# Performance work log

Hardware: AMD Instinct MI355X
Metric: run time of the kernel (lower is better)

Reference implementation:

```python
import jax, jax.numpy as jnp
import numpy as np

B, T, D = 4, 2048, 1024
H, DK = 8, 64
EPS = 1e-6

def _xavier(key, shape):
    fan_in, fan_out = shape[1], shape[0]
    lim = float(np.sqrt(6.0 / (fan_in + fan_out)))
    return jax.random.uniform(key, shape, jnp.float32, -lim, lim)

def setup_inputs() -> dict:
    key = jax.random.key(0)
    ks = jax.random.split(key, 7)
    x = jax.random.normal(ks[0], (B, T, D), jnp.float32)
    W_Q = _xavier(ks[1], (H * DK, D))
    W_K = _xavier(ks[2], (H * DK, D))
    W_V = _xavier(ks[3], (H * DK, D))
    W_g_w = _xavier(ks[4], (H * DK, D))
    W_g_b = jax.random.normal(ks[5], (H * DK,), jnp.float32) * 0.02
    W_O = _xavier(ks[6], (D, H * DK))
    decay_log = jnp.zeros((H,), jnp.float32)
    return {"x": x, "W_Q": W_Q, "W_K": W_K, "W_V": W_V,
            "W_g_w": W_g_w, "W_g_b": W_g_b, "W_O": W_O,
            "decay_log": decay_log}

def _phi(u):
    # ELU + 1 feature map (positive)
    return jax.nn.elu(u) + 1.0

def reference(x, W_Q, W_K, W_V, W_g_w, W_g_b, W_O, decay_log):
    b, t, d = x.shape
    q = _phi((x @ W_Q.T).reshape(b, t, H, DK))
    k = _phi((x @ W_K.T).reshape(b, t, H, DK))
    v = (x @ W_V.T).reshape(b, t, H, DK)
    gamma = jax.nn.sigmoid(decay_log)           # [H]
    g4 = gamma[None, :, None, None]             # [1,H,1,1]
    g3 = gamma[None, :, None]                   # [1,H,1]

    # time-major for scan: [T,B,H,DK]
    qT = jnp.moveaxis(q, 1, 0)
    kT = jnp.moveaxis(k, 1, 0)
    vT = jnp.moveaxis(v, 1, 0)

    S0 = jnp.zeros((b, H, DK, DK), x.dtype)
    z0 = jnp.zeros((b, H, DK), x.dtype)

    def step(carry, inp):
        S, z = carry
        qt, kt, vt = inp
        S = g4 * S + jnp.einsum('bhi,bhj->bhij', kt, vt)
        z = g3 * z + kt
        num = jnp.einsum('bhij,bhi->bhj', S, qt)
        den = jnp.sum(z * qt, axis=-1, keepdims=True) + EPS
        return (S, z), num / den

    _, ys = jax.lax.scan(step, (S0, z0), (qT, kT, vT))  # ys: [T,B,H,DK]
    outputs = jnp.moveaxis(ys, 0, 1)                    # [B,T,H,DK]

    gate = jax.nn.sigmoid(x @ W_g_w.T + W_g_b).reshape(b, t, H, DK)
    y = (outputs * gate).reshape(b, t, H * DK)
    return y @ W_O.T
```

## Files before the change

kernel.cpp:

```cpp
#include <hip/hip_runtime.h>
#include <cstdint>
#include <cstddef>

#define B_   4
#define T_   2048
#define D_   1024
#define H_   8
#define DK_  64
#define HD_  512
#define CH_  64
#define NC_  32
#define EPS_ 1e-6f

typedef __attribute__((ext_vector_type(4))) float f32x4;
typedef __attribute__((ext_vector_type(8))) short s16x8;

__device__ __forceinline__ unsigned short f2bf(float f) {
    unsigned int x = __float_as_uint(f);
    unsigned int r = (x + 0x7FFFu + ((x >> 16) & 1u)) >> 16;
    return (unsigned short)r;
}
__device__ __forceinline__ float bf2f(unsigned short u) {
    return __uint_as_float(((unsigned int)u) << 16);
}
__device__ __forceinline__ void ld4(const float* p, float* o) {
    float4 v = *(const float4*)p; o[0]=v.x; o[1]=v.y; o[2]=v.z; o[3]=v.w;
}

__global__ void k_f32_to_bf16(const float* __restrict__ in, unsigned short* __restrict__ out, int n4) {
    int i = blockIdx.x * blockDim.x + threadIdx.x;
    if (i < n4) {
        float4 v = ((const float4*)in)[i];
        ushort4 o;
        o.x = f2bf(v.x); o.y = f2bf(v.y); o.z = f2bf(v.z); o.w = f2bf(v.w);
        ((ushort4*)out)[i] = o;
    }
}

#define GT_M 128
#define GT_N 128
#define GBK  64
#define LDA  72

__global__ __launch_bounds__(256) void k_gemm_qkvg(
    const unsigned short* __restrict__ xb,
    const unsigned short* __restrict__ wqb, const unsigned short* __restrict__ wkb,
    const unsigned short* __restrict__ wvb, const unsigned short* __restrict__ wgb,
    const float* __restrict__ bias,
    unsigned short* __restrict__ qo, unsigned short* __restrict__ ko,
    unsigned short* __restrict__ vo, unsigned short* __restrict__ go)
{
    __shared__ unsigned short As[GT_M * LDA];
    __shared__ unsigned short Bs[GT_N * LDA];
    const int tid = threadIdx.x;
    const int which = blockIdx.x >> 2;
    const int nb    = blockIdx.x & 3;
    const int m0    = blockIdx.y * GT_M;
    const int n0    = nb * GT_N;
    const unsigned short* Wp = (which == 0) ? wqb : (which == 1) ? wkb : (which == 2) ? wvb : wgb;
    unsigned short* Op       = (which == 0) ? qo  : (which == 1) ? ko  : (which == 2) ? vo  : go;
    const int K = D_;

    const int lane = tid & 63, wave = tid >> 6;
    const int wm = (wave >> 1) * 64, wn = (wave & 1) * 64;
    const int r16 = lane & 15, quad = lane >> 4;

    f32x4 acc[4][4];
    #pragma unroll
    for (int a = 0; a < 4; a++)
        #pragma unroll
        for (int b = 0; b < 4; b++) acc[a][b] = 0.0f;

    for (int ko_ = 0; ko_ < K; ko_ += GBK) {
        #pragma unroll
        for (int i = 0; i < 4; i++) {
            int id = i * 256 + tid;
            int row = id >> 3, seg = id & 7;
            *(uint4*)&As[row * LDA + seg * 8] =
                *(const uint4*)(xb + (size_t)(m0 + row) * K + ko_ + seg * 8);
            *(uint4*)&Bs[row * LDA + seg * 8] =
                *(const uint4*)(Wp + (size_t)(n0 + row) * K + ko_ + seg * 8);
        }
        __syncthreads();
        #pragma unroll
        for (int kk = 0; kk < GBK; kk += 32) {
            s16x8 af[4], bf[4];
            #pragma unroll
            for (int mt = 0; mt < 4; mt++)
                af[mt] = *(const s16x8*)&As[(wm + mt * 16 + r16) * LDA + kk + quad * 8];
            #pragma unroll
            for (int nt = 0; nt < 4; nt++)
                bf[nt] = *(const s16x8*)&Bs[(wn + nt * 16 + r16) * LDA + kk + quad * 8];
            #pragma unroll
            for (int mt = 0; mt < 4; mt++)
                #pragma unroll
                for (int nt = 0; nt < 4; nt++)
                    acc[mt][nt] = __builtin_amdgcn_mfma_f32_16x16x32_bf16(af[mt], bf[nt], acc[mt][nt], 0, 0, 0);
        }
        __syncthreads();
    }
    #pragma unroll
    for (int mt = 0; mt < 4; mt++) {
        #pragma unroll
        for (int nt = 0; nt < 4; nt++) {
            int col = n0 + wn + nt * 16 + r16;
            float bv = (which == 3) ? bias[col] : 0.0f;
            #pragma unroll
            for (int r = 0; r < 4; r++) {
                int row = m0 + wm + mt * 16 + quad * 4 + r;
                float v = acc[mt][nt][r];
                if (which <= 1)      v = (v > 0.0f) ? v + 1.0f : __builtin_expf(v);
                else if (which == 3) v = 1.0f / (1.0f + __builtin_expf(-(v + bv)));
                Op[(size_t)row * HD_ + col] = f2bf(v);
            }
        }
    }
}

__global__ __launch_bounds__(256) void k_gemm_out(
    const unsigned short* __restrict__ ogb, const unsigned short* __restrict__ wob,
    float* __restrict__ y)
{
    __shared__ unsigned short As[GT_M * LDA];
    __shared__ unsigned short Bs[GT_N * LDA];
    const int tid = threadIdx.x;
    const int m0 = blockIdx.y * GT_M;
    const int n0 = blockIdx.x * GT_N;
    const int K = HD_;

    const int lane = tid & 63, wave = tid >> 6;
    const int wm = (wave >> 1) * 64, wn = (wave & 1) * 64;
    const int r16 = lane & 15, quad = lane >> 4;

    f32x4 acc[4][4];
    #pragma unroll
    for (int a = 0; a < 4; a++)
        #pragma unroll
        for (int b = 0; b < 4; b++) acc[a][b] = 0.0f;

    for (int ko_ = 0; ko_ < K; ko_ += GBK) {
        #pragma unroll
        for (int i = 0; i < 4; i++) {
            int id = i * 256 + tid;
            int row = id >> 3, seg = id & 7;
            *(uint4*)&As[row * LDA + seg * 8] =
                *(const uint4*)(ogb + (size_t)(m0 + row) * K + ko_ + seg * 8);
            *(uint4*)&Bs[row * LDA + seg * 8] =
                *(const uint4*)(wob + (size_t)(n0 + row) * K + ko_ + seg * 8);
        }
        __syncthreads();
        #pragma unroll
        for (int kk = 0; kk < GBK; kk += 32) {
            s16x8 af[4], bf[4];
            #pragma unroll
            for (int mt = 0; mt < 4; mt++)
                af[mt] = *(const s16x8*)&As[(wm + mt * 16 + r16) * LDA + kk + quad * 8];
            #pragma unroll
            for (int nt = 0; nt < 4; nt++)
                bf[nt] = *(const s16x8*)&Bs[(wn + nt * 16 + r16) * LDA + kk + quad * 8];
            #pragma unroll
            for (int mt = 0; mt < 4; mt++)
                #pragma unroll
                for (int nt = 0; nt < 4; nt++)
                    acc[mt][nt] = __builtin_amdgcn_mfma_f32_16x16x32_bf16(af[mt], bf[nt], acc[mt][nt], 0, 0, 0);
        }
        __syncthreads();
    }
    #pragma unroll
    for (int mt = 0; mt < 4; mt++)
        #pragma unroll
        for (int nt = 0; nt < 4; nt++) {
            int col = n0 + wn + nt * 16 + r16;
            #pragma unroll
            for (int r = 0; r < 4; r++) {
                int row = m0 + wm + mt * 16 + quad * 4 + r;
                y[(size_t)row * D_ + col] = acc[mt][nt][r];
            }
        }
}

__global__ __launch_bounds__(256) void k_chunk_sums(
    const unsigned short* __restrict__ Kb, const unsigned short* __restrict__ Vb,
    float* __restrict__ Ssum, float* __restrict__ zsum, const float* __restrict__ decay_log)
{
    __shared__ float kl[CH_ * 68];
    __shared__ float vl[CH_ * 68];
    const int tid = threadIdx.x;
    const int bc  = blockIdx.x;
    const int c   = bc & (NC_ - 1);
    const int bh  = bc >> 5;
    const int h   = bh & (H_ - 1);
    const int b   = bh >> 3;
    const float g  = 1.0f / (1.0f + __builtin_expf(-decay_log[h]));
    const float lg = __builtin_log2f(g);
    const int t0 = c * CH_;

    #pragma unroll
    for (int e = 0; e < 2; e++) {
        int lid = e * 256 + tid;
        int l = lid >> 3, d0 = (lid & 7) * 8;
        float w = __builtin_exp2f((float)(CH_ - 1 - l) * lg);
        size_t gidx = (size_t)(b * T_ + t0 + l) * HD_ + h * DK_ + d0;
        uint4 kraw = *(const uint4*)(Kb + gidx);
        uint4 vraw = *(const uint4*)(Vb + gidx);
        const unsigned short* kp = (const unsigned short*)&kraw;
        const unsigned short* vp = (const unsigned short*)&vraw;
        #pragma unroll
        for (int j = 0; j < 8; j++) {
            kl[l * 68 + d0 + j] = bf2f(kp[j]) * w;
            vl[l * 68 + d0 + j] = bf2f(vp[j]);
        }
    }
    __syncthreads();

    const int ti = tid >> 4, tj = tid & 15;
    const int i0 = ti * 4, j0 = tj * 4;
    float acc[4][4];
    #pragma unroll
    for (int r = 0; r < 4; r++)
        #pragma unroll
        for (int cc = 0; cc < 4; cc++) acc[r][cc] = 0.0f;

    for (int l = 0; l < CH_; l++) {
        float kv[4], vv[4];
        ld4(&kl[l * 68 + i0], kv);
        ld4(&vl[l * 68 + j0], vv);
        #pragma unroll
        for (int r = 0; r < 4; r++)
            #pragma unroll
            for (int cc = 0; cc < 4; cc++) acc[r][cc] += kv[r] * vv[cc];
    }
    size_t base = (size_t)bc * (DK_ * DK_);
    #pragma unroll
    for (int r = 0; r < 4; r++) {
        float4 st = make_float4(acc[r][0], acc[r][1], acc[r][2], acc[r][3]);
        *(float4*)&Ssum[base + (size_t)(i0 + r) * DK_ + j0] = st;
    }
    if (tid < DK_) {
        float s = 0.0f;
        for (int l = 0; l < CH_; l++) s += kl[l * 68 + tid];
        zsum[(size_t)bc * DK_ + tid] = s;
    }
}

__global__ __launch_bounds__(128) void k_chunk_scan(
    float* __restrict__ Ssum, float* __restrict__ zsum, const float* __restrict__ decay_log)
{
    const int tid = threadIdx.x;
    const int grp = blockIdx.x & 31;
    const int bh  = blockIdx.x >> 5;
    const int h   = bh & (H_ - 1);
    const float g  = 1.0f / (1.0f + __builtin_expf(-decay_log[h]));
    const float gC = __builtin_exp2f((float)CH_ * __builtin_log2f(g));
    int elem = grp * 128 + tid;
    float s = 0.0f;
    for (int c = 0; c < NC_; c++) {
        size_t idx = ((size_t)(bh * NC_ + c)) * 4096 + elem;
        float v = Ssum[idx];
        Ssum[idx] = s;
        s = gC * s + v;
    }
    if (grp == 0 && tid < DK_) {
        float z = 0.0f;
        for (int c = 0; c < NC_; c++) {
            size_t idx = ((size_t)(bh * NC_ + c)) * DK_ + tid;
            float v = zsum[idx];
            zsum[idx] = z;
            z = gC * z + v;
        }
    }
}

__global__ __launch_bounds__(256) void k_chunk_out(
    const unsigned short* __restrict__ Qb, const unsigned short* __restrict__ Kb,
    const unsigned short* __restrict__ Vb, const unsigned short* __restrict__ Gb,
    const float* __restrict__ Ssum, const float* __restrict__ zsum,
    unsigned short* __restrict__ OGb, const float* __restrict__ decay_log)
{
    __shared__ float BufA[CH_ * 68];
    __shared__ float BufB[CH_ * 68];
    __shared__ float BufC[CH_ * 68];
    __shared__ float den_l[CH_];
    __shared__ float zp_l[DK_];
    __shared__ float gpow[CH_ + 1];

    const int tid = threadIdx.x;
    const int bc  = blockIdx.x;
    const int c   = bc & (NC_ - 1);
    const int bh  = bc >> 5;
    const int h   = bh & (H_ - 1);
    const int b   = bh >> 3;
    const float g  = 1.0f / (1.0f + __builtin_expf(-decay_log[h]));
    const float lg = __builtin_log2f(g);
    const int t0 = c * CH_;

    if (tid <= CH_) gpow[tid] = __builtin_exp2f((float)tid * lg);
    if (tid < DK_)  zp_l[tid] = zsum[(size_t)bc * DK_ + tid];

    #pragma unroll
    for (int e = 0; e < 2; e++) {
        int lid = e * 256 + tid;
        int l = lid >> 3, d0 = (lid & 7) * 8;
        size_t gidx = (size_t)(b * T_ + t0 + l) * HD_ + h * DK_ + d0;
        uint4 qraw = *(const uint4*)(Qb + gidx);
        uint4 kraw = *(const uint4*)(Kb + gidx);
        const unsigned short* qp = (const unsigned short*)&qraw;
        const unsigned short* kp = (const unsigned short*)&kraw;
        #pragma unroll
        for (int j = 0; j < 8; j++) {
            BufA[(d0 + j) * 68 + l] = bf2f(qp[j]);
            BufB[(d0 + j) * 68 + l] = bf2f(kp[j]);
        }
    }
    {
        size_t base = (size_t)bc * 4096;
        #pragma unroll
        for (int e = 0; e < 4; e++) {
            int flat = (e * 256 + tid) * 4;
            int row = flat >> 6, c0 = flat & 63;
            *(float4*)&BufC[row * 68 + c0] = *(const float4*)&Ssum[base + flat];
        }
    }
    __syncthreads();

    const int ti = tid >> 4, tj = tid & 15;
    const int i0 = ti * 4, j0 = tj * 4;
    float sc[4][4], it[4][4];
    #pragma unroll
    for (int r = 0; r < 4; r++)
        #pragma unroll
        for (int cc = 0; cc < 4; cc++) { sc[r][cc] = 0.0f; it[r][cc] = 0.0f; }

    for (int d = 0; d < DK_; d++) {
        float qv[4], kv[4], sv[4];
        ld4(&BufA[d * 68 + i0], qv);
        ld4(&BufB[d * 68 + j0], kv);
        ld4(&BufC[d * 68 + j0], sv);
        #pragma unroll
        for (int r = 0; r < 4; r++)
            #pragma unroll
            for (int cc = 0; cc < 4; cc++) {
                sc[r][cc] += qv[r] * kv[cc];
                it[r][cc] += qv[r] * sv[cc];
            }
    }
    #pragma unroll
    for (int r = 0; r < 4; r++) {
        int i = i0 + r;
        #pragma unroll
        for (int cc = 0; cc < 4; cc++) {
            int jl = j0 + cc;
            sc[r][cc] = (jl <= i) ? sc[r][cc] * gpow[i - jl] : 0.0f;
            it[r][cc] *= gpow[i + 1];
        }
        float rs = sc[r][0] + sc[r][1] + sc[r][2] + sc[r][3];
        rs += __shfl_xor(rs, 1);
        rs += __shfl_xor(rs, 2);
        rs += __shfl_xor(rs, 4);
        rs += __shfl_xor(rs, 8);
        if (tj == 0) den_l[i] = rs;
    }
    __syncthreads();
    if (tid < DK_) {
        float dp = 0.0f;
        for (int d = 0; d < DK_; d++) dp += BufA[d * 68 + tid] * zp_l[d];
        den_l[tid] += gpow[tid + 1] * dp + EPS_;
    }
    __syncthreads();
    #pragma unroll
    for (int cc = 0; cc < 4; cc++) {
        float4 st = make_float4(sc[0][cc], sc[1][cc], sc[2][cc], sc[3][cc]);
        *(float4*)&BufA[(j0 + cc) * 68 + i0] = st;
    }
    #pragma unroll
    for (int e = 0; e < 2; e++) {
        int lid = e * 256 + tid;
        int l = lid >> 3, d0 = (lid & 7) * 8;
        size_t gidx = (size_t)(b * T_ + t0 + l) * HD_ + h * DK_ + d0;
        uint4 vraw = *(const uint4*)(Vb + gidx);
        const unsigned short* vp = (const unsigned short*)&vraw;
        #pragma unroll
        for (int j = 0; j < 8; j++) BufB[l * 68 + d0 + j] = bf2f(vp[j]);
    }
    __syncthreads();

    float og[4][4];
    #pragma unroll
    for (int r = 0; r < 4; r++)
        #pragma unroll
        for (int cc = 0; cc < 4; cc++) og[r][cc] = it[r][cc];

    for (int jl = 0; jl < CH_; jl++) {
        float scv[4], vv[4];
        ld4(&BufA[jl * 68 + i0], scv);
        ld4(&BufB[jl * 68 + j0], vv);
        #pragma unroll
        for (int r = 0; r < 4; r++)
            #pragma unroll
            for (int cc = 0; cc < 4; cc++) og[r][cc] += scv[r] * vv[cc];
    }
    #pragma unroll
    for (int r = 0; r < 4; r++) {
        int i = i0 + r;
        float rcp = 1.0f / den_l[i];
        size_t gidx = (size_t)(b * T_ + t0 + i) * HD_ + h * DK_ + j0;
        ushort4 graw = *(const ushort4*)(Gb + gidx);
        ushort4 o;
        o.x = f2bf(og[r][0] * rcp * bf2f(graw.x));
        o.y = f2bf(og[r][1] * rcp * bf2f(graw.y));
        o.z = f2bf(og[r][2] * rcp * bf2f(graw.z));
        o.w = f2bf(og[r][3] * rcp * bf2f(graw.w));
        *(ushort4*)(OGb + gidx) = o;
    }
}

extern "C" void kernel_launch(void* const* d_in, const int* in_sizes, int n_in,
                              void* d_out, int out_size, void* d_ws, size_t ws_size,
                              hipStream_t stream)
{
    (void)in_sizes; (void)n_in; (void)out_size; (void)ws_size;
    const float* x         = (const float*)d_in[0];
    const float* W_Q       = (const float*)d_in[1];
    const float* W_K       = (const float*)d_in[2];
    const float* W_V       = (const float*)d_in[3];
    const float* W_gw      = (const float*)d_in[4];
    const float* W_gb      = (const float*)d_in[5];
    const float* W_O       = (const float*)d_in[6];
    const float* decay_log = (const float*)d_in[7];
    float* y = (float*)d_out;

    char* ws = (char*)d_ws;
    size_t off = 0;
    auto alloc = [&](size_t bytes) { void* p = ws + off; off += (bytes + 255) & ~(size_t)255; return p; };
    unsigned short* xb   = (unsigned short*)alloc((size_t)B_ * T_ * D_ * 2);
    unsigned short* wqb  = (unsigned short*)alloc((size_t)HD_ * D_ * 2);
    unsigned short* wkb  = (unsigned short*)alloc((size_t)HD_ * D_ * 2);
    unsigned short* wvb  = (unsigned short*)alloc((size_t)HD_ * D_ * 2);
    unsigned short* wgb  = (unsigned short*)alloc((size_t)HD_ * D_ * 2);
    unsigned short* wob  = (unsigned short*)alloc((size_t)D_ * HD_ * 2);
    unsigned short* qb   = (unsigned short*)alloc((size_t)B_ * T_ * HD_ * 2);
    unsigned short* kb   = (unsigned short*)alloc((size_t)B_ * T_ * HD_ * 2);
    unsigned short* vb   = (unsigned short*)alloc((size_t)B_ * T_ * HD_ * 2);
    unsigned short* gb   = (unsigned short*)alloc((size_t)B_ * T_ * HD_ * 2);
    unsigned short* ogb  = (unsigned short*)alloc((size_t)B_ * T_ * HD_ * 2);
    float* Ssum = (float*)alloc((size_t)B_ * H_ * NC_ * DK_ * DK_ * 4);
    float* zsum = (float*)alloc((size_t)B_ * H_ * NC_ * DK_ * 4);

    int n4;
    n4 = B_ * T_ * D_ / 4;
    k_f32_to_bf16<<<(n4 + 255) / 256, 256, 0, stream>>>(x, xb, n4);
    n4 = HD_ * D_ / 4;
    k_f32_to_bf16<<<(n4 + 255) / 256, 256, 0, stream>>>(W_Q,  wqb, n4);
    k_f32_to_bf16<<<(n4 + 255) / 256, 256, 0, stream>>>(W_K,  wkb, n4);
    k_f32_to_bf16<<<(n4 + 255) / 256, 256, 0, stream>>>(W_V,  wvb, n4);
    k_f32_to_bf16<<<(n4 + 255) / 256, 256, 0, stream>>>(W_gw, wgb, n4);
    k_f32_to_bf16<<<(n4 + 255) / 256, 256, 0, stream>>>(W_O,  wob, n4);

    k_gemm_qkvg<<<dim3(16, 64), 256, 0, stream>>>(xb, wqb, wkb, wvb, wgb, W_gb, qb, kb, vb, gb);
    k_chunk_sums<<<B_ * H_ * NC_, 256, 0, stream>>>(kb, vb, Ssum, zsum, decay_log);
    k_chunk_scan<<<B_ * H_ * NC_, 128, 0, stream>>>(Ssum, zsum, decay_log);
    k_chunk_out<<<B_ * H_ * NC_, 256, 0, stream>>>(qb, kb, vb, gb, Ssum, zsum, ogb, decay_log);
    k_gemm_out<<<dim3(8, 64), 256, 0, stream>>>(ogb, wob, y);
}
```

Before: 233.4 us.

## Merge bf16 conversions into one launch and use direct global-to-LDS loads in GEMMs

Six separate fp32-to-bf16 conversion launches are replaced by a single kernel that picks its source and destination by block index, removing launch overhead. Both GEMM kernels now fill shared-memory tiles with global_load_lds (direct global-to-LDS transfers) instead of a register round trip. To allow this, the LDS row stride drops from 72 to 64, which removes the padding and may bring back bank conflicts on the MFMA fragment reads.

```diff
diff --git a/kernel.cpp b/kernel.cpp
--- a/kernel.cpp
+++ b/kernel.cpp
@@ -26,21 +26,48 @@
 __device__ __forceinline__ void ld4(const float* p, float* o) {
     float4 v = *(const float4*)p; o[0]=v.x; o[1]=v.y; o[2]=v.z; o[3]=v.w;
 }
-
-__global__ void k_f32_to_bf16(const float* __restrict__ in, unsigned short* __restrict__ out, int n4) {
-    int i = blockIdx.x * blockDim.x + threadIdx.x;
-    if (i < n4) {
-        float4 v = ((const float4*)in)[i];
-        ushort4 o;
-        o.x = f2bf(v.x); o.y = f2bf(v.y); o.z = f2bf(v.z); o.w = f2bf(v.w);
-        ((ushort4*)out)[i] = o;
-    }
+__device__ __forceinline__ void gl_lds16(const unsigned short* g, unsigned short* l) {
+    __builtin_amdgcn_global_load_lds(
+        (const __attribute__((address_space(1))) unsigned int*)g,
+        (__attribute__((address_space(3))) unsigned int*)l, 16, 0, 0);
+}
+
+__global__ __launch_bounds__(256) void k_cvt_all(
+    const float* __restrict__ x,
+    const float* __restrict__ wq, const float* __restrict__ wk,
+    const float* __restrict__ wv, const float* __restrict__ wgw,
+    const float* __restrict__ wo,
+    unsigned short* __restrict__ xb,
+    unsigned short* __restrict__ wqb, unsigned short* __restrict__ wkb,
+    unsigned short* __restrict__ wvb, unsigned short* __restrict__ wgb,
+    unsigned short* __restrict__ wob)
+{
+    int bid = blockIdx.x;
+    const float* src; unsigned short* dst; int idx;
+    if (bid < 8192) {
+        src = x; dst = xb; idx = bid * 256 + threadIdx.x;
+    } else {
+        int r = bid - 8192;
+        int w = r >> 9;
+        idx = (r & 511) * 256 + threadIdx.x;
+        switch (w) {
+            case 0:  src = wq;  dst = wqb; break;
+            case 1:  src = wk;  dst = wkb; break;
+            case 2:  src = wv;  dst = wvb; break;
+            case 3:  src = wgw; dst = wgb; break;
+            default: src = wo;  dst = wob; break;
+        }
+    }
+    float4 v = ((const float4*)src)[idx];
+    ushort4 o;
+    o.x = f2bf(v.x); o.y = f2bf(v.y); o.z = f2bf(v.z); o.w = f2bf(v.w);
+    ((ushort4*)dst)[idx] = o;
 }
 
 #define GT_M 128
 #define GT_N 128
 #define GBK  64
-#define LDA  72
+#define LDA  64
 
 __global__ __launch_bounds__(256) void k_gemm_qkvg(
     const unsigned short* __restrict__ xb,
@@ -64,6 +91,7 @@
     const int lane = tid & 63, wave = tid >> 6;
     const int wm = (wave >> 1) * 64, wn = (wave & 1) * 64;
     const int r16 = lane & 15, quad = lane >> 4;
+    const int lrow = lane >> 3, lseg = lane & 7;
 
     f32x4 acc[4][4];
     #pragma unroll
@@ -74,12 +102,10 @@
     for (int ko_ = 0; ko_ < K; ko_ += GBK) {
         #pragma unroll
         for (int i = 0; i < 4; i++) {
-            int id = i * 256 + tid;
-            int row = id >> 3, seg = id & 7;
-            *(uint4*)&As[row * LDA + seg * 8] =
-                *(const uint4*)(xb + (size_t)(m0 + row) * K + ko_ + seg * 8);
-            *(uint4*)&Bs[row * LDA + seg * 8] =
-                *(const uint4*)(Wp + (size_t)(n0 + row) * K + ko_ + seg * 8);
+            int chunk = wave * 4 + i;
+            int row = chunk * 8 + lrow;
+            gl_lds16(xb + (size_t)(m0 + row) * K + ko_ + lseg * 8, As + chunk * 512);
+            gl_lds16(Wp + (size_t)(n0 + row) * K + ko_ + lseg * 8, Bs + chunk * 512);
         }
         __syncthreads();
         #pragma unroll
@@ -131,6 +157,7 @@
     const int lane = tid & 63, wave = tid >> 6;
     const int wm = (wave >> 1) * 64, wn = (wave & 1) * 64;
     const int r16 = lane & 15, quad = lane >> 4;
+    const int lrow = lane >> 3, lseg = lane & 7;
 
     f32x4 acc[4][4];
     #pragma unroll
@@ -141,12 +168,10 @@
     for (int ko_ = 0; ko_ < K; ko_ += GBK) {
         #pragma unroll
         for (int i = 0; i < 4; i++) {
-            int id = i * 256 + tid;
-            int row = id >> 3, seg = id & 7;
-            *(uint4*)&As[row * LDA + seg * 8] =
-                *(const uint4*)(ogb + (size_t)(m0 + row) * K + ko_ + seg * 8);
-            *(uint4*)&Bs[row * LDA + seg * 8] =
-                *(const uint4*)(wob + (size_t)(n0 + row) * K + ko_ + seg * 8);
+            int chunk = wave * 4 + i;
+            int row = chunk * 8 + lrow;
+            gl_lds16(ogb + (size_t)(m0 + row) * K + ko_ + lseg * 8, As + chunk * 512);
+            gl_lds16(wob + (size_t)(n0 + row) * K + ko_ + lseg * 8, Bs + chunk * 512);
         }
         __syncthreads();
         #pragma unroll
@@ -446,16 +471,8 @@
     float* Ssum = (float*)alloc((size_t)B_ * H_ * NC_ * DK_ * DK_ * 4);
     float* zsum = (float*)alloc((size_t)B_ * H_ * NC_ * DK_ * 4);
 
-    int n4;
-    n4 = B_ * T_ * D_ / 4;
-    k_f32_to_bf16<<<(n4 + 255) / 256, 256, 0, stream>>>(x, xb, n4);
-    n4 = HD_ * D_ / 4;
-    k_f32_to_bf16<<<(n4 + 255) / 256, 256, 0, stream>>>(W_Q,  wqb, n4);
-    k_f32_to_bf16<<<(n4 + 255) / 256, 256, 0, stream>>>(W_K,  wkb, n4);
-    k_f32_to_bf16<<<(n4 + 255) / 256, 256, 0, stream>>>(W_V,  wvb, n4);
-    k_f32_to_bf16<<<(n4 + 255) / 256, 256, 0, stream>>>(W_gw, wgb, n4);
-    k_f32_to_bf16<<<(n4 + 255) / 256, 256, 0, stream>>>(W_O,  wob, n4);
-
+    k_cvt_all<<<8192 + 5 * 512, 256, 0, stream>>>(x, W_Q, W_K, W_V, W_gw, W_O,
+                                                  xb, wqb, wkb, wvb, wgb, wob);
     k_gemm_qkvg<<<dim3(16, 64), 256, 0, stream>>>(xb, wqb, wkb, wvb, wgb, W_gb, qb, kb, vb, gb);
     k_chunk_sums<<<B_ * H_ * NC_, 256, 0, stream>>>(kb, vb, Ssum, zsum, decay_log);
     k_chunk_scan<<<B_ * H_ * NC_, 128, 0, stream>>>(Ssum, zsum, decay_log);
```

After: 232.6 us. No clear change (-0.3%).
